# Kernel tuning notes

Hardware: AMD Instinct MI355X
Metric: run time of the kernel (lower is better)

The kernel has to match this reference:

```python
import jax, jax.numpy as jnp
import numpy as np

TAU_U = 1.0
TAU_L = 0.05
EPS = 1e-12  # torch F.normalize eps


def setup_inputs() -> dict:
    key = jax.random.key(0)
    ks = jax.random.split(key, 8)
    N, D, B = 100000, 128, 8192
    x1 = jax.random.normal(ks[0], (N, D), dtype=jnp.float32)
    x2 = jax.random.normal(ks[1], (N, D), dtype=jnp.float32)
    x1_index = jax.random.randint(ks[2], (B,), 0, N, dtype=jnp.int64 if jax.config.jax_enable_x64 else jnp.int32)
    x2_index = jax.random.randint(ks[3], (B,), 0, N, dtype=jnp.int64 if jax.config.jax_enable_x64 else jnp.int32)
    # Linear params (torch Linear default init: U(-1/sqrt(fan_in), 1/sqrt(fan_in)))
    lim1 = 1.0 / np.sqrt(D)
    W1 = jax.random.uniform(ks[4], (D, D), minval=-lim1, maxval=lim1, dtype=jnp.float32)
    b1 = jax.random.uniform(ks[5], (D,), minval=-lim1, maxval=lim1, dtype=jnp.float32)
    W2 = jax.random.uniform(ks[6], (1, D), minval=-lim1, maxval=lim1, dtype=jnp.float32)
    b2 = jax.random.uniform(ks[7], (1,), minval=-lim1, maxval=lim1, dtype=jnp.float32)
    return {"x1": x1, "x2": x2, "x1_index": x1_index, "x2_index": x2_index,
            "W1": W1, "b1": b1, "W2": W2, "b2": b2}


def _l2norm(x):
    # matches torch F.normalize(dim=1) for 2-D input
    n = jnp.sqrt(jnp.sum(x * x, axis=-1, keepdims=True))
    return x / jnp.maximum(n, EPS)


def reference(x1, x2, x1_index, x2_index, W1, b1, W2, b2):
    x1_feat = _l2norm(x1[x1_index])          # [B, D]
    x2_feat = _l2norm(x2[x2_index])          # [B, D]

    h = x1_feat * x2_feat                    # [B, D]
    h = h @ W1.T + b1                        # lin1
    h = jnp.where(h >= 0, h, 0.2 * h)        # leaky_relu(0.2)
    s = jax.nn.sigmoid(h @ W2.T + b2)        # [B, 1]
    ssl_temp = (TAU_U - TAU_L) * (1.0 - s) + TAU_L   # [B, 1]

    pos = jnp.sum(x1_feat * x2_feat, axis=-1)         # [B]
    # NOTE: [B] / [B,1] broadcasts to [B,B] exactly like torch
    pos_rating = jnp.exp(pos / ssl_temp)              # [B, B]

    tot = x1_feat @ x2_feat.T                          # [B, B]
    tot_rating = jnp.sum(jnp.exp(tot / ssl_temp), axis=1)  # [B]

    ssl_temp_avg = jnp.mean(ssl_temp)
    return (pos_rating, tot_rating, ssl_temp_avg)
```

## Files before the change

kernel.cpp:

```cpp
#include <hip/hip_runtime.h>
#include <stdint.h>

typedef __bf16 bf16x8 __attribute__((ext_vector_type(8)));
typedef float f32x4 __attribute__((ext_vector_type(4)));
typedef __attribute__((address_space(3))) uint32_t as3u32;
typedef const __attribute__((address_space(1))) uint32_t as1u32;

#define B_TOT 8192
#define DD 128
#define OUT_TOT 67108864UL
#define OUT_AVG 67117056UL

__device__ inline unsigned short f2bf(float x){
  union { float f; uint32_t u; } v; v.f = x;
  return (unsigned short)((v.u + 0x7fffu + ((v.u >> 16) & 1u)) >> 16);
}

__device__ inline float bsum128(float v, volatile float* s2){
  #pragma unroll
  for (int o = 32; o; o >>= 1) v += __shfl_xor(v, o);
  __syncthreads();
  if ((threadIdx.x & 63) == 0) s2[threadIdx.x >> 6] = v;
  __syncthreads();
  return s2[0] + s2[1];
}

__global__ __launch_bounds__(128) void k_feat(const float* __restrict__ x1,
    const float* __restrict__ x2, const int* __restrict__ i1a, const int* __restrict__ i2a,
    unsigned short* __restrict__ f1b, unsigned short* __restrict__ f2b,
    unsigned short* __restrict__ hb, float* __restrict__ posw, float* __restrict__ out){
  __shared__ float s2[2];
  int b = blockIdx.x, t = threadIdx.x;
  int gid = b * 128 + t;
  if (gid <= 8192) out[OUT_TOT + gid] = 0.f;
  size_t r1 = (size_t)i1a[b] * DD, r2 = (size_t)i2a[b] * DD;
  float v1 = x1[r1 + t], v2 = x2[r2 + t];
  float n1 = sqrtf(bsum128(v1 * v1, s2));
  float f1 = v1 / fmaxf(n1, 1e-12f);
  float n2 = sqrtf(bsum128(v2 * v2, s2));
  float f2 = v2 / fmaxf(n2, 1e-12f);
  float h = f1 * f2;
  float pos = bsum128(h, s2);
  int o = b * DD + t;
  f1b[o] = f2bf(f1); f2b[o] = f2bf(f2); hb[o] = f2bf(h);
  if (t == 0) posw[b] = pos;
}

__device__ inline void stage_tile(const unsigned short* g, unsigned short* s){
  int tid = threadIdx.x;
  #pragma unroll
  for (int it = 0; it < 8; ++it){
    int c = tid + it * 256;
    int row = c >> 4, cc = c & 15;
    int src = (row << 4) + (cc ^ (row & 7));
    __builtin_amdgcn_global_load_lds((as1u32*)(g + src * 8),
                                     (as3u32*)(s + c * 8), 16, 0, 0);
  }
}

__device__ inline void mfma_tile(const unsigned short* As, const unsigned short* Bs,
                                 f32x4 acc[4][4]){
  int tid = threadIdx.x;
  int w = tid >> 6, l = tid & 63;
  int wr = (w >> 1) * 64, wc = (w & 1) * 64;
  int lo = l & 15, hi = l >> 4;
  f32x4 zero = {0.f, 0.f, 0.f, 0.f};
  #pragma unroll
  for (int m = 0; m < 4; ++m)
    #pragma unroll
    for (int n = 0; n < 4; ++n) acc[m][n] = zero;
  #pragma unroll
  for (int kk = 0; kk < 4; ++kk){
    bf16x8 af[4], bfv[4];
    #pragma unroll
    for (int m = 0; m < 4; ++m){
      int row = wr + m * 16 + lo;
      af[m] = *(const bf16x8*)(As + row * 128 + ((kk * 4 + hi) ^ (row & 7)) * 8);
    }
    #pragma unroll
    for (int n = 0; n < 4; ++n){
      int row = wc + n * 16 + lo;
      bfv[n] = *(const bf16x8*)(Bs + row * 128 + ((kk * 4 + hi) ^ (row & 7)) * 8);
    }
    #pragma unroll
    for (int m = 0; m < 4; ++m)
      #pragma unroll
      for (int n = 0; n < 4; ++n)
        acc[m][n] = __builtin_amdgcn_mfma_f32_16x16x32_bf16(af[m], bfv[n], acc[m][n], 0, 0, 0);
  }
}

__global__ __launch_bounds__(256) void k_lin(const unsigned short* __restrict__ hb,
    const float* __restrict__ W1, const float* __restrict__ b1,
    const float* __restrict__ W2, const float* __restrict__ b2,
    float* __restrict__ rTw, float* __restrict__ out){
  __shared__ __align__(16) unsigned short As[16384];
  __shared__ __align__(16) unsigned short Bs[16384];
  __shared__ float zpart[2][128];
  __shared__ float s4[4];
  int i0 = blockIdx.x * 128;
  int tid = threadIdx.x;
  stage_tile(hb + (size_t)i0 * 128, As);
  #pragma unroll
  for (int it = 0; it < 8; ++it){
    int c = tid + it * 256;
    int row = c >> 4, cc = c & 15;
    int src = (row << 4) + (cc ^ (row & 7));
    const float4* g4 = (const float4*)(W1 + src * 8);
    float4 a = g4[0], b = g4[1];
    unsigned short t8[8];
    t8[0] = f2bf(a.x); t8[1] = f2bf(a.y); t8[2] = f2bf(a.z); t8[3] = f2bf(a.w);
    t8[4] = f2bf(b.x); t8[5] = f2bf(b.y); t8[6] = f2bf(b.z); t8[7] = f2bf(b.w);
    *(uint4*)(Bs + c * 8) = *(uint4*)t8;
  }
  asm volatile("s_waitcnt vmcnt(0)" ::: "memory");
  __syncthreads();
  f32x4 acc[4][4];
  mfma_tile(As, Bs, acc);
  int w = tid >> 6, l = tid & 63;
  int wrb = (w >> 1) * 64, wcb = (w & 1) * 64, lo = l & 15, hi = l >> 4;
  float w2v[4], b1v[4];
  #pragma unroll
  for (int n = 0; n < 4; ++n){ int col = wcb + n * 16 + lo; w2v[n] = W2[col]; b1v[n] = b1[col]; }
  #pragma unroll
  for (int m = 0; m < 4; ++m){
    #pragma unroll
    for (int q = 0; q < 4; ++q){
      float p = 0.f;
      #pragma unroll
      for (int n = 0; n < 4; ++n){
        float hv = acc[m][n][q] + b1v[n];
        hv = hv >= 0.f ? hv : 0.2f * hv;
        p += hv * w2v[n];
      }
      p += __shfl_xor(p, 1); p += __shfl_xor(p, 2);
      p += __shfl_xor(p, 4); p += __shfl_xor(p, 8);
      if (lo == 0) zpart[w & 1][wrb + m * 16 + hi * 4 + q] = p;
    }
  }
  __syncthreads();
  float Tloc = 0.f;
  if (tid < 128){
    float z = zpart[0][tid] + zpart[1][tid] + b2[0];
    float s = 1.f / (1.f + __expf(-z));
    float T = 0.95f * (1.f - s) + 0.05f;
    rTw[i0 + tid] = 1.f / T;
    Tloc = T;
  }
  float v = Tloc;
  #pragma unroll
  for (int o = 32; o; o >>= 1) v += __shfl_xor(v, o);
  if ((tid & 63) == 0) s4[tid >> 6] = v;
  __syncthreads();
  if (tid == 0) atomicAdd(out + OUT_AVG, (s4[0] + s4[1] + s4[2] + s4[3]) * (1.0f / 8192.0f));
}

__global__ __launch_bounds__(256, 2) void k_tot(const unsigned short* __restrict__ f1b,
    const unsigned short* __restrict__ f2b, const float* __restrict__ rTw,
    const float* __restrict__ posw, float* __restrict__ out){
  __shared__ __align__(16) unsigned short Buf[16384];
  __shared__ __align__(16) float posS[1024];
  __shared__ __align__(16) float rS[128];
  int s = (blockIdx.x & 7) * 64 + (blockIdx.x >> 3);
  int rt = s & 63, ctg = s >> 6;
  int tid = threadIdx.x, w = tid >> 6, l = tid & 63;
  int wr = (w >> 1) * 64, wc = (w & 1) * 64;
  int lo = l & 15, hi = l >> 4;
  stage_tile(f1b + (size_t)rt * 16384, Buf);
  __builtin_amdgcn_global_load_lds((as1u32*)(posw + ctg * 1024 + tid * 4),
                                   (as3u32*)(posS + tid * 4), 16, 0, 0);
  if (tid < 32)
    __builtin_amdgcn_global_load_lds((as1u32*)(rTw + rt * 128 + tid * 4),
                                     (as3u32*)(rS + tid * 4), 16, 0, 0);
  asm volatile("s_waitcnt vmcnt(0)" ::: "memory");
  __builtin_amdgcn_s_barrier();
  bf16x8 af[4][4];
  #pragma unroll
  for (int kk = 0; kk < 4; ++kk)
    #pragma unroll
    for (int m = 0; m < 4; ++m){
      int row = wr + m * 16 + lo;
      af[kk][m] = *(const bf16x8*)(Buf + row * 128 + ((kk * 4 + hi) ^ (row & 7)) * 8);
    }
  asm volatile("s_waitcnt lgkmcnt(0)" ::: "memory");
  __builtin_amdgcn_s_barrier();
  stage_tile(f2b + (size_t)(ctg * 8) * 16384, Buf);
  asm volatile("s_waitcnt vmcnt(0)" ::: "memory");
  __builtin_amdgcn_s_barrier();
  float pacc[4][4] = {{0.f,0.f,0.f,0.f},{0.f,0.f,0.f,0.f},{0.f,0.f,0.f,0.f},{0.f,0.f,0.f,0.f}};
  int prow = tid >> 5, pcol = (tid & 31) * 4;
  #pragma unroll 1
  for (int c8 = 0; c8 < 8; ++c8){
    int ct = ctg * 8 + c8;
    f32x4 acc[4][4];
    f32x4 zero = {0.f,0.f,0.f,0.f};
    #pragma unroll
    for (int m = 0; m < 4; ++m)
      #pragma unroll
      for (int n = 0; n < 4; ++n) acc[m][n] = zero;
    #pragma unroll
    for (int kk = 0; kk < 4; ++kk){
      bf16x8 bfv[4];
      #pragma unroll
      for (int n = 0; n < 4; ++n){
        int row = wc + n * 16 + lo;
        bfv[n] = *(const bf16x8*)(Buf + row * 128 + ((kk * 4 + hi) ^ (row & 7)) * 8);
      }
      #pragma unroll
      for (int m = 0; m < 4; ++m)
        #pragma unroll
        for (int n = 0; n < 4; ++n)
          acc[m][n] = __builtin_amdgcn_mfma_f32_16x16x32_bf16(af[kk][m], bfv[n], acc[m][n], 0, 0, 0);
    }
    asm volatile("s_waitcnt lgkmcnt(0)" ::: "memory");
    __builtin_amdgcn_s_barrier();
    if (c8 < 7) stage_tile(f2b + (size_t)(ct + 1) * 16384, Buf);
    __builtin_amdgcn_sched_barrier(0);
    #pragma unroll
    for (int m = 0; m < 4; ++m)
      #pragma unroll
      for (int q = 0; q < 4; ++q){
        float r = rS[wr + m * 16 + hi * 4 + q];
        pacc[m][q] += __expf(acc[m][0][q] * r) + __expf(acc[m][1][q] * r)
                    + __expf(acc[m][2][q] * r) + __expf(acc[m][3][q] * r);
      }
    f32x4 p4 = *(const f32x4*)&posS[c8 * 128 + pcol];
    float* obase = out + (size_t)(rt * 128) * B_TOT + ct * 128 + pcol;
    #pragma unroll
    for (int pass = 0; pass < 16; ++pass){
      int row = pass * 8 + prow;
      float r = rS[row];
      f32x4 e;
      e.x = __expf(p4.x * r); e.y = __expf(p4.y * r);
      e.z = __expf(p4.z * r); e.w = __expf(p4.w * r);
      __builtin_nontemporal_store(e, (f32x4*)(obase + (size_t)row * B_TOT));
    }
    if (c8 < 7){
      asm volatile("s_waitcnt vmcnt(16)" ::: "memory");
      __builtin_amdgcn_s_barrier();
    }
  }
  #pragma unroll
  for (int m = 0; m < 4; ++m)
    #pragma unroll
    for (int q = 0; q < 4; ++q){
      float p = pacc[m][q];
      p += __shfl_xor(p, 1); p += __shfl_xor(p, 2);
      p += __shfl_xor(p, 4); p += __shfl_xor(p, 8);
      if (lo == 0) atomicAdd(out + OUT_TOT + rt * 128 + wr + m * 16 + hi * 4 + q, p);
    }
}

extern "C" void kernel_launch(void* const* d_in, const int* in_sizes, int n_in,
                              void* d_out, int out_size, void* d_ws, size_t ws_size,
                              hipStream_t stream){
  const float* x1 = (const float*)d_in[0];
  const float* x2 = (const float*)d_in[1];
  const int*   i1 = (const int*)d_in[2];
  const int*   i2 = (const int*)d_in[3];
  const float* W1 = (const float*)d_in[4];
  const float* b1 = (const float*)d_in[5];
  const float* W2 = (const float*)d_in[6];
  const float* b2 = (const float*)d_in[7];
  float* out = (float*)d_out;
  char* ws = (char*)d_ws;
  unsigned short* hb   = (unsigned short*)(ws);
  unsigned short* f1b  = (unsigned short*)(ws + 2097152);
  unsigned short* f2b  = (unsigned short*)(ws + 4194304);
  float* posw  = (float*)(ws + 6291456);
  float* rTw   = (float*)(ws + 6324224);

  hipLaunchKernelGGL(k_feat,  dim3(8192), dim3(128), 0, stream, x1, x2, i1, i2, f1b, f2b, hb, posw, out);
  hipLaunchKernelGGL(k_lin,   dim3(64),   dim3(256), 0, stream, hb, W1, b1, W2, b2, rTw, out);
  hipLaunchKernelGGL(k_tot,   dim3(512),  dim3(256), 0, stream, f1b, f2b, rTw, posw, out);
}
```

Baseline: 92.02 us.

## Use one wavefront per row in feat kernel and write full pos_rating rows

The feature kernel now handles one batch row per 64-lane wavefront with float2 loads and shuffle-only reductions. This removes the shared-memory block reductions and their barriers and packs the bf16 outputs into 32-bit stores. In the tot kernel, each block now writes 16 complete rows of the [B,B] pos_rating output instead of a 128x128 tile of strided rows, so stores are long contiguous runs. In exchange, every block loads all of posw (32KB) into LDS, which raises LDS use and may reduce occupancy under the 2-blocks-per-CU launch bound.

Result: faster. 87.41 us (-5.0%).

```diff
diff --git a/kernel.cpp b/kernel.cpp
--- a/kernel.cpp
+++ b/kernel.cpp
@@ -16,34 +16,37 @@
   return (unsigned short)((v.u + 0x7fffu + ((v.u >> 16) & 1u)) >> 16);
 }
 
-__device__ inline float bsum128(float v, volatile float* s2){
-  #pragma unroll
-  for (int o = 32; o; o >>= 1) v += __shfl_xor(v, o);
-  __syncthreads();
-  if ((threadIdx.x & 63) == 0) s2[threadIdx.x >> 6] = v;
-  __syncthreads();
-  return s2[0] + s2[1];
-}
-
-__global__ __launch_bounds__(128) void k_feat(const float* __restrict__ x1,
+__global__ __launch_bounds__(256) void k_feat(const float* __restrict__ x1,
     const float* __restrict__ x2, const int* __restrict__ i1a, const int* __restrict__ i2a,
     unsigned short* __restrict__ f1b, unsigned short* __restrict__ f2b,
     unsigned short* __restrict__ hb, float* __restrict__ posw, float* __restrict__ out){
-  __shared__ float s2[2];
-  int b = blockIdx.x, t = threadIdx.x;
-  int gid = b * 128 + t;
+  int tid = threadIdx.x;
+  int gid = blockIdx.x * 256 + tid;
   if (gid <= 8192) out[OUT_TOT + gid] = 0.f;
-  size_t r1 = (size_t)i1a[b] * DD, r2 = (size_t)i2a[b] * DD;
-  float v1 = x1[r1 + t], v2 = x2[r2 + t];
-  float n1 = sqrtf(bsum128(v1 * v1, s2));
-  float f1 = v1 / fmaxf(n1, 1e-12f);
-  float n2 = sqrtf(bsum128(v2 * v2, s2));
-  float f2 = v2 / fmaxf(n2, 1e-12f);
-  float h = f1 * f2;
-  float pos = bsum128(h, s2);
-  int o = b * DD + t;
-  f1b[o] = f2bf(f1); f2b[o] = f2bf(f2); hb[o] = f2bf(h);
-  if (t == 0) posw[b] = pos;
+  int w = tid >> 6, l = tid & 63;
+  int b = blockIdx.x * 4 + w;
+  const float2* r1 = (const float2*)(x1 + (size_t)i1a[b] * DD);
+  const float2* r2 = (const float2*)(x2 + (size_t)i2a[b] * DD);
+  float2 v1 = r1[l], v2 = r2[l];
+  float s1 = v1.x * v1.x + v1.y * v1.y;
+  float s2 = v2.x * v2.x + v2.y * v2.y;
+  #pragma unroll
+  for (int o = 32; o; o >>= 1){ s1 += __shfl_xor(s1, o); s2 += __shfl_xor(s2, o); }
+  float inv1 = 1.f / fmaxf(sqrtf(s1), 1e-12f);
+  float inv2 = 1.f / fmaxf(sqrtf(s2), 1e-12f);
+  float f1x = v1.x * inv1, f1y = v1.y * inv1;
+  float f2x = v2.x * inv2, f2y = v2.y * inv2;
+  float hx = f1x * f2x, hy = f1y * f2y;
+  float ps = hx + hy;
+  #pragma unroll
+  for (int o = 32; o; o >>= 1) ps += __shfl_xor(ps, o);
+  unsigned int u1 = (unsigned int)f2bf(f1x) | ((unsigned int)f2bf(f1y) << 16);
+  unsigned int u2 = (unsigned int)f2bf(f2x) | ((unsigned int)f2bf(f2y) << 16);
+  unsigned int uh = (unsigned int)f2bf(hx)  | ((unsigned int)f2bf(hy)  << 16);
+  ((unsigned int*)f1b)[b * 64 + l] = u1;
+  ((unsigned int*)f2b)[b * 64 + l] = u2;
+  ((unsigned int*)hb)[b * 64 + l]  = uh;
+  if (l == 0) posw[b] = ps;
 }
 
 __device__ inline void stage_tile(const unsigned short* g, unsigned short* s){
@@ -159,19 +162,27 @@
     const unsigned short* __restrict__ f2b, const float* __restrict__ rTw,
     const float* __restrict__ posw, float* __restrict__ out){
   __shared__ __align__(16) unsigned short Buf[16384];
-  __shared__ __align__(16) float posS[1024];
+  __shared__ __align__(16) float posS[8192];
   __shared__ __align__(16) float rS[128];
+  __shared__ __align__(16) float rQ[16];
   int s = (blockIdx.x & 7) * 64 + (blockIdx.x >> 3);
   int rt = s & 63, ctg = s >> 6;
   int tid = threadIdx.x, w = tid >> 6, l = tid & 63;
   int wr = (w >> 1) * 64, wc = (w & 1) * 64;
   int lo = l & 15, hi = l >> 4;
   stage_tile(f1b + (size_t)rt * 16384, Buf);
-  __builtin_amdgcn_global_load_lds((as1u32*)(posw + ctg * 1024 + tid * 4),
-                                   (as3u32*)(posS + tid * 4), 16, 0, 0);
+  #pragma unroll
+  for (int it = 0; it < 8; ++it){
+    int c = tid + it * 256;
+    __builtin_amdgcn_global_load_lds((as1u32*)(posw + c * 4),
+                                     (as3u32*)(posS + c * 4), 16, 0, 0);
+  }
   if (tid < 32)
     __builtin_amdgcn_global_load_lds((as1u32*)(rTw + rt * 128 + tid * 4),
                                      (as3u32*)(rS + tid * 4), 16, 0, 0);
+  if (tid < 4)
+    __builtin_amdgcn_global_load_lds((as1u32*)(rTw + s * 16 + tid * 4),
+                                     (as3u32*)(rQ + tid * 4), 16, 0, 0);
   asm volatile("s_waitcnt vmcnt(0)" ::: "memory");
   __builtin_amdgcn_s_barrier();
   bf16x8 af[4][4];
@@ -188,7 +199,7 @@
   asm volatile("s_waitcnt vmcnt(0)" ::: "memory");
   __builtin_amdgcn_s_barrier();
   float pacc[4][4] = {{0.f,0.f,0.f,0.f},{0.f,0.f,0.f,0.f},{0.f,0.f,0.f,0.f},{0.f,0.f,0.f,0.f}};
-  int prow = tid >> 5, pcol = (tid & 31) * 4;
+  int half = w & 1, rsel = w >> 1;
   #pragma unroll 1
   for (int c8 = 0; c8 < 8; ++c8){
     int ct = ctg * 8 + c8;
@@ -224,16 +235,18 @@
         pacc[m][q] += __expf(acc[m][0][q] * r) + __expf(acc[m][1][q] * r)
                     + __expf(acc[m][2][q] * r) + __expf(acc[m][3][q] * r);
       }
-    f32x4 p4 = *(const f32x4*)&posS[c8 * 128 + pcol];
-    float* obase = out + (size_t)(rt * 128) * B_TOT + ct * 128 + pcol;
-    #pragma unroll
-    for (int pass = 0; pass < 16; ++pass){
-      int row = pass * 8 + prow;
-      float r = rS[row];
-      f32x4 e;
-      e.x = __expf(p4.x * r); e.y = __expf(p4.y * r);
-      e.z = __expf(p4.z * r); e.w = __expf(p4.w * r);
-      __builtin_nontemporal_store(e, (f32x4*)(obase + (size_t)row * B_TOT));
+    {
+      int rowi = s * 16 + c8 * 2 + rsel;
+      float rr = rQ[c8 * 2 + rsel];
+      float* obase = out + (size_t)rowi * B_TOT + half * 4096;
+      #pragma unroll
+      for (int j = 0; j < 16; ++j){
+        f32x4 p = *(const f32x4*)&posS[half * 4096 + j * 256 + l * 4];
+        f32x4 e;
+        e.x = __expf(p.x * rr); e.y = __expf(p.y * rr);
+        e.z = __expf(p.z * rr); e.w = __expf(p.w * rr);
+        __builtin_nontemporal_store(e, (f32x4*)(obase + j * 256 + l * 4));
+      }
     }
     if (c8 < 7){
       asm volatile("s_waitcnt vmcnt(16)" ::: "memory");
@@ -270,7 +283,7 @@
   float* posw  = (float*)(ws + 6291456);
   float* rTw   = (float*)(ws + 6324224);
 
-  hipLaunchKernelGGL(k_feat,  dim3(8192), dim3(128), 0, stream, x1, x2, i1, i2, f1b, f2b, hb, posw, out);
+  hipLaunchKernelGGL(k_feat,  dim3(2048), dim3(256), 0, stream, x1, x2, i1, i2, f1b, f2b, hb, posw, out);
   hipLaunchKernelGGL(k_lin,   dim3(64),   dim3(256), 0, stream, hb, W1, b1, W2, b2, rTw, out);
   hipLaunchKernelGGL(k_tot,   dim3(512),  dim3(256), 0, stream, f1b, f2b, rTw, posw, out);
 }
```
